# Kernel tuning notes

Hardware: AMD Instinct MI355X
Metric: run time of the kernel (lower is better)

## Reference

```python
import jax, jax.numpy as jnp
import numpy as np

EPS = 1e-5

def binarize(x):
    # binarize11: sign to {-1,+1} (0 maps to +1)
    return jnp.where(x >= 0, 1.0, -1.0).astype(x.dtype)

def batchnorm_train(x, gamma, beta):
    # training-mode BatchNorm1D: batch statistics over axis 0
    mean = jnp.mean(x, axis=0)
    var = jnp.var(x, axis=0)
    return gamma * (x - mean) * jax.lax.rsqrt(var + EPS) + beta

def setup_inputs() -> dict:
    key = jax.random.key(0)
    ks = jax.random.split(key, 16)
    x = jax.random.uniform(ks[0], (65536, 784), dtype=jnp.float32)  # MNIST-like pixels in [0,1]
    shapes = [(256, 784), (256, 256), (256, 256), (256, 256), (10, 256)]
    inp = {"x": x}
    for i, (o, ii) in enumerate(shapes):
        inp[f"w{i}"] = jax.random.normal(ks[1 + i], (o, ii), dtype=jnp.float32) * 0.05
        inp[f"gamma{i}"] = jnp.ones((o,), dtype=jnp.float32)
        inp[f"beta{i}"] = jnp.zeros((o,), dtype=jnp.float32)
    return inp

def reference(x, w0, w1, w2, w3, w4, gamma0, gamma1, gamma2, gamma3, gamma4,
              beta0, beta1, beta2, beta3, beta4):
    ws = [w0, w1, w2, w3, w4]
    gs = [gamma0, gamma1, gamma2, gamma3, gamma4]
    bs = [beta0, beta1, beta2, beta3, beta4]
    out = x - 0.5
    for k in range(5):
        a = binarize(out)                 # binarize activations
        wb = binarize(ws[k])              # binarize weights
        out = a @ wb.T                    # [B, out_k]
        out = batchnorm_train(out, gs[k], bs[k])
    # faithful to original: Softmax(dim=0) = softmax over the BATCH axis
    return jax.nn.softmax(out, axis=0)
```

## Files before the change

### kernel.cpp

```cpp
#include <hip/hip_runtime.h>
#include <cstdint>
#include <climits>
#include <cstddef>

typedef unsigned long long u64;

#define B_ROWS 65536
#define BN_EPS 1e-5


__global__ __launch_bounds__(256) void prep_all(
    const float* __restrict__ x, const float* __restrict__ w0,
    const float* __restrict__ w1, const float* __restrict__ w2,
    const float* __restrict__ w3, const float* __restrict__ w4,
    u64* __restrict__ bitsx, u64* __restrict__ wb0p, u64* __restrict__ wbTp,
    u64* __restrict__ w4b,
    long long* gsum, long long* gsq, int* gmin, int* gmax, double* colsum)
{
    const int lane = threadIdx.x & 63;
    const int wv   = threadIdx.x >> 6;
    const int b    = blockIdx.x;

    if (b < 2048) {
        const int gw = b * 4 + wv;
        for (int i = 0; i < 8; ++i) {
            const int row = gw * 8 + i;
            const float4* xr = (const float4*)(x + (size_t)row * 784);
#pragma unroll
            for (int cg = 0; cg < 3; ++cg) {
                const float4 f = xr[cg*64 + lane];
                const u64 e0 = __ballot(f.x >= 0.5f);
                const u64 e1 = __ballot(f.y >= 0.5f);
                const u64 e2 = __ballot(f.z >= 0.5f);
                const u64 e3 = __ballot(f.w >= 0.5f);
                if (lane == 0) {
                    bitsx[(size_t)(cg*4+0)*65536 + row] = e0;
                    bitsx[(size_t)(cg*4+1)*65536 + row] = e1;
                    bitsx[(size_t)(cg*4+2)*65536 + row] = e2;
                    bitsx[(size_t)(cg*4+3)*65536 + row] = e3;
                }
            }
            float4 f = make_float4(-1.f, -1.f, -1.f, -1.f);
            if (lane < 4) f = xr[192 + lane];
            const u64 e0 = __ballot(f.x >= 0.5f) & 0xF;
            const u64 e1 = __ballot(f.y >= 0.5f) & 0xF;
            const u64 e2 = __ballot(f.z >= 0.5f) & 0xF;
            const u64 e3 = __ballot(f.w >= 0.5f) & 0xF;
            if (lane == 0)
                bitsx[(size_t)12*65536 + row] = e0 | (e1 << 4) | (e2 << 8) | (e3 << 12);
        }
    } else if (b < 2112) {
        const int c = (b - 2048) * 4 + wv;
        const int pb = (c & 7) * 13;
        const int g  = c >> 3;
        const float4* row = (const float4*)(w0 + (size_t)c * 784);
#pragma unroll
        for (int cg = 0; cg < 3; ++cg) {
            const float4 f = row[cg*64 + lane];
            const u64 e0 = __ballot(f.x >= 0.0f);
            const u64 e1 = __ballot(f.y >= 0.0f);
            const u64 e2 = __ballot(f.z >= 0.0f);
            const u64 e3 = __ballot(f.w >= 0.0f);
            if (lane == 0) {
                wb0p[(pb + cg*4+0)*32 + g] = e0;
                wb0p[(pb + cg*4+1)*32 + g] = e1;
                wb0p[(pb + cg*4+2)*32 + g] = e2;
                wb0p[(pb + cg*4+3)*32 + g] = e3;
            }
        }
        float4 f = make_float4(-1.f, -1.f, -1.f, -1.f);
        if (lane < 4) f = row[192 + lane];
        const u64 e0 = __ballot(f.x >= 0.0f) & 0xF;
        const u64 e1 = __ballot(f.y >= 0.0f) & 0xF;
        const u64 e2 = __ballot(f.z >= 0.0f) & 0xF;
        const u64 e3 = __ballot(f.w >= 0.0f) & 0xF;
        if (lane == 0) wb0p[(pb + 12)*32 + g] = e0 | (e1 << 4) | (e2 << 8) | (e3 << 12);
    } else if (b < 2307) {
        const int idx = (b - 2112) * 4 + wv;
        if (idx < 768) {
            const int L = idx >> 8, c = idx & 255;
            const float* ws = (L == 0) ? w1 : (L == 1) ? w2 : w3;
            const float4 f = *(const float4*)(ws + (size_t)c * 256 + 4*lane);
            const u64 e0 = __ballot(f.x >= 0.0f);
            const u64 e1 = __ballot(f.y >= 0.0f);
            const u64 e2 = __ballot(f.z >= 0.0f);
            const u64 e3 = __ballot(f.w >= 0.0f);
            if (lane == 0) {
                const int pb = (c & 7) * 4;
                const int g  = c >> 3;
                wbTp[L*1024 + (pb+0)*32 + g] = e0;
                wbTp[L*1024 + (pb+1)*32 + g] = e1;
                wbTp[L*1024 + (pb+2)*32 + g] = e2;
                wbTp[L*1024 + (pb+3)*32 + g] = e3;
            }
        } else if (idx < 778) {
            const int c = idx - 768;
            const float4 f = *(const float4*)(w4 + (size_t)c * 256 + 4*lane);
            const u64 e0 = __ballot(f.x >= 0.0f);
            const u64 e1 = __ballot(f.y >= 0.0f);
            const u64 e2 = __ballot(f.z >= 0.0f);
            const u64 e3 = __ballot(f.w >= 0.0f);
            if (lane == 0) {
                w4b[c*4+0] = e0; w4b[c*4+1] = e1; w4b[c*4+2] = e2; w4b[c*4+3] = e3;
            }
        }
    } else {
        for (int i = threadIdx.x; i < 1040; i += 256) { gsum[i] = 0; gsq[i] = 0; }
        if (threadIdx.x < 16) {
            gmin[threadIdx.x] = INT_MAX;
            gmax[threadIdx.x] = INT_MIN;
            colsum[threadIdx.x] = 0.0;
        }
    }
}

__device__ __forceinline__ void bn_threshold(long long sv, long long qv,
    float gaf, float bef, int& sg, int& t)
{
    const double mean = (double)sv / (double)B_ROWS;
    double var = (double)qv / (double)B_ROWS - mean * mean;
    if (var < 0.0) var = 0.0;
    const double rs    = 1.0 / sqrt(var + BN_EPS);
    const double scale = (double)gaf * rs;
    const double bt    = (double)bef;
    if (scale > 0.0) {
        const double tt = fmin(fmax(mean - bt / scale, -1e6), 1e6);
        sg = 1; t = (int)ceil(tt);
    } else if (scale < 0.0) {
        const double tt = fmin(fmax(mean - bt / scale, -1e6), 1e6);
        sg = -1; t = (int)(-floor(tt));
    } else { sg = 0; t = (bt >= 0.0) ? INT_MIN : 1; }
}

template<int KW>
__device__ __forceinline__ void gemm_coal(const u64* __restrict__ sA,
    const u64* __restrict__ sWp, int K, int row0,
    short* __restrict__ vout, long long* gsumL, long long* gsqL,
    int* sS, int* sQ)
{
    const int tid = threadIdx.x;
    const int ct  = tid & 31;
    const int rt  = tid >> 5;

    unsigned p2[8][4];
#pragma unroll
    for (int j = 0; j < 8; ++j)
#pragma unroll
        for (int e2 = 0; e2 < 4; ++e2) p2[j][e2] = 0;

#pragma unroll 1
    for (int k = 0; k < KW; ++k) {
        u64 a[8];
#pragma unroll
        for (int j = 0; j < 8; ++j) a[j] = sA[k*128 + rt + 16*j];
        u64 w[8];
#pragma unroll
        for (int e = 0; e < 8; ++e) w[e] = sWp[(e*KW + k)*32 + ct];
#pragma unroll
        for (int j = 0; j < 8; ++j)
#pragma unroll
            for (int e2 = 0; e2 < 4; ++e2)
                p2[j][e2] += (unsigned)__popcll(a[j] ^ w[2*e2])
                           + ((unsigned)__popcll(a[j] ^ w[2*e2+1]) << 16);
    }

    int sS8[8], sQ8[8];
#pragma unroll
    for (int e = 0; e < 8; ++e) { sS8[e] = 0; sQ8[e] = 0; }

#pragma unroll
    for (int j = 0; j < 8; ++j) {
        const int r = row0 + rt + 16*j;
        unsigned pk[4];
#pragma unroll
        for (int e2 = 0; e2 < 4; ++e2) {
            const int v0 = K - 2 * (int)(p2[j][e2] & 0xFFFFu);
            const int v1 = K - 2 * (int)(p2[j][e2] >> 16);
            sS8[2*e2]   += v0; sQ8[2*e2]   += v0*v0;
            sS8[2*e2+1] += v1; sQ8[2*e2+1] += v1*v1;
            pk[e2] = (unsigned)(unsigned short)(short)v0
                   | ((unsigned)(unsigned short)(short)v1 << 16);
        }
        *(uint4*)(vout + (size_t)r * 256 + 8*ct) = make_uint4(pk[0], pk[1], pk[2], pk[3]);
    }

#pragma unroll
    for (int e = 0; e < 8; ++e) {
        sS8[e] += __shfl_xor(sS8[e], 32);
        sQ8[e] += __shfl_xor(sQ8[e], 32);
    }
    if ((tid & 63) < 32) {
#pragma unroll
        for (int e = 0; e < 8; ++e) {
            atomicAdd(&sS[8*ct + e], sS8[e]);
            atomicAdd(&sQ[8*ct + e], sQ8[e]);
        }
    }
    __syncthreads();
    if (tid < 256) {
        atomicAdd((u64*)&gsumL[tid], (u64)(long long)sS[tid]);
        atomicAdd((u64*)&gsqL[tid],  (u64)(long long)sQ[tid]);
    }
}

__global__ __launch_bounds__(512, 4) void layer0_kernel(
    const u64* __restrict__ bitsx, const u64* __restrict__ wb0p,
    short* __restrict__ v, long long* gsum, long long* gsq)
{
    __shared__ __align__(16) u64 sA[13*128];
    __shared__ __align__(16) u64 sWp[13*8*32];
    __shared__ int sS[256], sQ[256];
    const int tid  = threadIdx.x;
    const int row0 = blockIdx.x * 128;
    for (int i = tid; i < 13*128; i += 512)
        sA[i] = bitsx[(size_t)(i >> 7)*65536 + row0 + (i & 127)];
    for (int i = tid; i < 13*8*32; i += 512) sWp[i] = wb0p[i];
    if (tid < 256) { sS[tid] = 0; sQ[tid] = 0; }
    __syncthreads();
    gemm_coal<13>(sA, sWp, 784, row0, v, gsum, gsq, sS, sQ);
}

__global__ __launch_bounds__(512, 4) void layer_mid_kernel(
    short* v,
    const long long* __restrict__ gsumP, const long long* __restrict__ gsqP,
    const float* __restrict__ gaP, const float* __restrict__ beP,
    const u64* __restrict__ wbTpL, long long* gsumC, long long* gsqC)
{
    __shared__ __align__(16) u64 sA[4*128];
    __shared__ __align__(16) u64 sWp[4*8*32];
    __shared__ int sSgn[256], sThr[256];
    __shared__ int sS[256], sQ[256];
    const int tid  = threadIdx.x;
    const int lane = tid & 63;
    const int wv   = tid >> 6;
    const int row0 = blockIdx.x * 128;

    for (int i = tid; i < 4*8*32; i += 512) sWp[i] = wbTpL[i];
    if (tid < 256) {
        int sg, t;
        bn_threshold(gsumP[tid], gsqP[tid], gaP[tid], beP[tid], sg, t);
        sSgn[tid] = sg; sThr[tid] = t;
        sS[tid] = 0; sQ[tid] = 0;
    }
    __syncthreads();

    const int4 sg4 = *(const int4*)&sSgn[4*lane];
    const int4 th4 = *(const int4*)&sThr[4*lane];
    for (int i = 0; i < 16; ++i) {
        const int r = wv * 16 + i;
        const short4 vv = *(const short4*)(v + (size_t)(row0 + r)*256 + 4*lane);
        const u64 e0 = __ballot(sg4.x * (int)vv.x >= th4.x);
        const u64 e1 = __ballot(sg4.y * (int)vv.y >= th4.y);
        const u64 e2 = __ballot(sg4.z * (int)vv.z >= th4.z);
        const u64 e3 = __ballot(sg4.w * (int)vv.w >= th4.w);
        if (lane == 0) {
            sA[0*128 + r] = e0; sA[1*128 + r] = e1;
            sA[2*128 + r] = e2; sA[3*128 + r] = e3;
        }
    }
    __syncthreads();
    gemm_coal<4>(sA, sWp, 256, row0, v, gsumC, gsqC, sS, sQ);
}

__global__ __launch_bounds__(512) void layer4_kernel(
    const short* __restrict__ v,
    const long long* __restrict__ gsumP, const long long* __restrict__ gsqP,
    const float* __restrict__ gaP, const float* __restrict__ beP,
    const u64* __restrict__ w4b, short* __restrict__ v4,
    long long* gsum4, long long* gsq4, int* gmin, int* gmax)
{
    __shared__ int sSgn[256], sThr[256];
    __shared__ int sS[10], sQ[10], sMn[10], sMx[10];
    const int tid  = threadIdx.x;
    const int lane = tid & 63;
    const int wv   = tid >> 6;

    if (tid < 256) {
        int sg, t;
        bn_threshold(gsumP[tid], gsqP[tid], gaP[tid], beP[tid], sg, t);
        sSgn[tid] = sg; sThr[tid] = t;
    }
    if (tid < 10) { sS[tid] = 0; sQ[tid] = 0; sMn[tid] = INT_MAX; sMx[tid] = INT_MIN; }
    __syncthreads();

    const int4 sg4 = *(const int4*)&sSgn[4*lane];
    const int4 th4 = *(const int4*)&sThr[4*lane];

    u64 wc0 = 0, wc1 = 0, wc2 = 0, wc3 = 0;
    if (lane < 10) {
        wc0 = w4b[lane*4+0]; wc1 = w4b[lane*4+1];
        wc2 = w4b[lane*4+2]; wc3 = w4b[lane*4+3];
    }

    int accS = 0, accQ = 0, mn = INT_MAX, mx = INT_MIN;
    const int waveId = blockIdx.x * 8 + wv;
    const int r0 = waveId * 16;
#pragma unroll 2
    for (int i = 0; i < 16; ++i) {
        const int r = r0 + i;
        const short4 vv = *(const short4*)(v + (size_t)r*256 + 4*lane);
        const u64 e0 = __ballot(sg4.x * (int)vv.x >= th4.x);
        const u64 e1 = __ballot(sg4.y * (int)vv.y >= th4.y);
        const u64 e2 = __ballot(sg4.z * (int)vv.z >= th4.z);
        const u64 e3 = __ballot(sg4.w * (int)vv.w >= th4.w);
        if (lane < 10) {
            const int p = (int)__popcll(e0 ^ wc0) + (int)__popcll(e1 ^ wc1)
                        + (int)__popcll(e2 ^ wc2) + (int)__popcll(e3 ^ wc3);
            const int vr = 256 - 2*p;
            v4[(size_t)r*10 + lane] = (short)vr;
            accS += vr; accQ += vr*vr;
            mn = min(mn, vr); mx = max(mx, vr);
        }
    }
    if (lane < 10) {
        atomicAdd(&sS[lane], accS);
        atomicAdd(&sQ[lane], accQ);
        atomicMin(&sMn[lane], mn);
        atomicMax(&sMx[lane], mx);
    }
    __syncthreads();
    if (tid < 10) {
        atomicAdd((u64*)&gsum4[tid], (u64)(long long)sS[tid]);
        atomicAdd((u64*)&gsq4[tid],  (u64)(long long)sQ[tid]);
        atomicMin(&gmin[tid], sMn[tid]);
        atomicMax(&gmax[tid], sMx[tid]);
    }
}

__global__ __launch_bounds__(256) void colsum_kernel(
    const short* __restrict__ v4,
    const long long* __restrict__ gsum4, const long long* __restrict__ gsq4,
    const int* __restrict__ gmin, const int* __restrict__ gmax,
    const float* __restrict__ g4, const float* __restrict__ b4,
    double* zsg, double* zbg, double* colsum)
{
    __shared__ double sred[256];
    __shared__ double sZ[2];
    const int c     = blockIdx.x % 10;
    const int chunk = blockIdx.x / 10;
    const int tid   = threadIdx.x;
    if (tid == 0) {
        const double mean = (double)gsum4[c] / (double)B_ROWS;
        double var = (double)gsq4[c] / (double)B_ROWS - mean * mean;
        if (var < 0.0) var = 0.0;
        const double rs    = 1.0 / sqrt(var + BN_EPS);
        const double scale = (double)g4[c] * rs;
        const double bias  = (double)b4[c] - mean * scale;
        const double z1 = scale * (double)gmin[c] + bias;
        const double z2 = scale * (double)gmax[c] + bias;
        const double zb = bias - fmax(z1, z2);
        sZ[0] = scale; sZ[1] = zb;
        zsg[c] = scale; zbg[c] = zb;
    }
    __syncthreads();
    const double zs = sZ[0], zb = sZ[1];
    double acc = 0.0;
    const int r0 = chunk * 1024;
#pragma unroll
    for (int j = 0; j < 4; ++j) {
        const int r = r0 + j*256 + tid;
        acc += exp(zs * (double)v4[(size_t)r*10 + c] + zb);
    }
    sred[tid] = acc; __syncthreads();
    for (int s = 128; s > 0; s >>= 1) {
        if (tid < s) sred[tid] += sred[tid + s];
        __syncthreads();
    }
    if (tid == 0) atomicAdd(&colsum[c], sred[0]);
}

__global__ __launch_bounds__(256) void out_kernel(
    const short* __restrict__ v4, const double* __restrict__ zsg,
    const double* __restrict__ zbg, const double* __restrict__ colsum,
    float* __restrict__ out)
{
    const int idx = blockIdx.x * 256 + threadIdx.x;
    if (idx >= B_ROWS * 10) return;
    const int c = idx % 10;
    out[idx] = (float)(exp(zsg[c] * (double)v4[idx] + zbg[c]) / colsum[c]);
}

extern "C" void kernel_launch(void* const* d_in, const int* in_sizes, int n_in,
                              void* d_out, int out_size, void* d_ws, size_t ws_size,
                              hipStream_t stream)
{
    const float* x  = (const float*)d_in[0];
    const float* w0 = (const float*)d_in[1];
    const float* g0 = (const float*)d_in[2];
    const float* b0 = (const float*)d_in[3];
    const float* w1 = (const float*)d_in[4];
    const float* g1 = (const float*)d_in[5];
    const float* b1 = (const float*)d_in[6];
    const float* w2 = (const float*)d_in[7];
    const float* g2 = (const float*)d_in[8];
    const float* b2 = (const float*)d_in[9];
    const float* w3 = (const float*)d_in[10];
    const float* g3 = (const float*)d_in[11];
    const float* b3 = (const float*)d_in[12];
    const float* w4 = (const float*)d_in[13];
    const float* g4 = (const float*)d_in[14];
    const float* b4 = (const float*)d_in[15];

    char* p = (char*)d_ws;
    auto alloc = [&](size_t bytes) -> char* {
        char* r = p;
        p += (bytes + 255) & ~(size_t)255;
        return r;
    };
    u64*       bitsx  = (u64*)alloc(13ull*65536*8);
    u64*       wb0p   = (u64*)alloc(13*8*32*8);
    u64*       wbTp   = (u64*)alloc(3*1024*8);
    u64*       w4b    = (u64*)alloc(40*8);
    short*     v      = (short*)alloc(65536ull*256*2);
    short*     v4     = (short*)alloc(65536ull*10*2);
    long long* gsum   = (long long*)alloc(1040*8);
    long long* gsq    = (long long*)alloc(1040*8);
    int*       gmin   = (int*)alloc(16*4);
    int*       gmax   = (int*)alloc(16*4);
    double*    colsum = (double*)alloc(16*8);
    double*    zsg    = (double*)alloc(16*8);
    double*    zbg    = (double*)alloc(16*8);
    float*     out    = (float*)d_out;

    long long* gsum4 = gsum + 1024;
    long long* gsq4  = gsq  + 1024;

    prep_all<<<2308, 256, 0, stream>>>(x, w0, w1, w2, w3, w4,
                                       bitsx, wb0p, wbTp, w4b,
                                       gsum, gsq, gmin, gmax, colsum);

    layer0_kernel<<<512, 512, 0, stream>>>(bitsx, wb0p, v, gsum, gsq);

    layer_mid_kernel<<<512, 512, 0, stream>>>(v, gsum, gsq, g0, b0,
                                              wbTp + 0*1024, gsum + 256, gsq + 256);
    layer_mid_kernel<<<512, 512, 0, stream>>>(v, gsum + 256, gsq + 256, g1, b1,
                                              wbTp + 1*1024, gsum + 512, gsq + 512);
    layer_mid_kernel<<<512, 512, 0, stream>>>(v, gsum + 512, gsq + 512, g2, b2,
                                              wbTp + 2*1024, gsum + 768, gsq + 768);

    layer4_kernel<<<512, 512, 0, stream>>>(v, gsum + 768, gsq + 768, g3, b3,
                                           w4b, v4, gsum4, gsq4, gmin, gmax);

    colsum_kernel<<<640, 256, 0, stream>>>(v4, gsum4, gsq4, gmin, gmax, g4, b4,
                                           zsg, zbg, colsum);

    out_kernel<<<2560, 256, 0, stream>>>(v4, zsg, zbg, colsum, out);
}
```

Before: 207.3 us.

## Fuse input binarization into layer0 GEMM and shrink blocks to 32 rows

```diff
diff --git a/kernel.cpp b/kernel.cpp
--- a/kernel.cpp
+++ b/kernel.cpp
@@ -9,48 +9,19 @@
 #define BN_EPS 1e-5
 
 
-__global__ __launch_bounds__(256) void prep_all(
-    const float* __restrict__ x, const float* __restrict__ w0,
-    const float* __restrict__ w1, const float* __restrict__ w2,
-    const float* __restrict__ w3, const float* __restrict__ w4,
-    u64* __restrict__ bitsx, u64* __restrict__ wb0p, u64* __restrict__ wbTp,
-    u64* __restrict__ w4b,
+__global__ __launch_bounds__(256) void prep_w(
+    const float* __restrict__ w0, const float* __restrict__ w1,
+    const float* __restrict__ w2, const float* __restrict__ w3,
+    const float* __restrict__ w4,
+    u64* __restrict__ wb0p, u64* __restrict__ wbTp, u64* __restrict__ w4b,
     long long* gsum, long long* gsq, int* gmin, int* gmax, double* colsum)
 {
     const int lane = threadIdx.x & 63;
     const int wv   = threadIdx.x >> 6;
     const int b    = blockIdx.x;
 
-    if (b < 2048) {
-        const int gw = b * 4 + wv;
-        for (int i = 0; i < 8; ++i) {
-            const int row = gw * 8 + i;
-            const float4* xr = (const float4*)(x + (size_t)row * 784);
-#pragma unroll
-            for (int cg = 0; cg < 3; ++cg) {
-                const float4 f = xr[cg*64 + lane];
-                const u64 e0 = __ballot(f.x >= 0.5f);
-                const u64 e1 = __ballot(f.y >= 0.5f);
-                const u64 e2 = __ballot(f.z >= 0.5f);
-                const u64 e3 = __ballot(f.w >= 0.5f);
-                if (lane == 0) {
-                    bitsx[(size_t)(cg*4+0)*65536 + row] = e0;
-                    bitsx[(size_t)(cg*4+1)*65536 + row] = e1;
-                    bitsx[(size_t)(cg*4+2)*65536 + row] = e2;
-                    bitsx[(size_t)(cg*4+3)*65536 + row] = e3;
-                }
-            }
-            float4 f = make_float4(-1.f, -1.f, -1.f, -1.f);
-            if (lane < 4) f = xr[192 + lane];
-            const u64 e0 = __ballot(f.x >= 0.5f) & 0xF;
-            const u64 e1 = __ballot(f.y >= 0.5f) & 0xF;
-            const u64 e2 = __ballot(f.z >= 0.5f) & 0xF;
-            const u64 e3 = __ballot(f.w >= 0.5f) & 0xF;
-            if (lane == 0)
-                bitsx[(size_t)12*65536 + row] = e0 | (e1 << 4) | (e2 << 8) | (e3 << 12);
-        }
-    } else if (b < 2112) {
-        const int c = (b - 2048) * 4 + wv;
+    if (b < 64) {
+        const int c  = b * 4 + wv;
         const int pb = (c & 7) * 13;
         const int g  = c >> 3;
         const float4* row = (const float4*)(w0 + (size_t)c * 784);
@@ -75,33 +46,33 @@
         const u64 e2 = __ballot(f.z >= 0.0f) & 0xF;
         const u64 e3 = __ballot(f.w >= 0.0f) & 0xF;
         if (lane == 0) wb0p[(pb + 12)*32 + g] = e0 | (e1 << 4) | (e2 << 8) | (e3 << 12);
-    } else if (b < 2307) {
-        const int idx = (b - 2112) * 4 + wv;
-        if (idx < 768) {
-            const int L = idx >> 8, c = idx & 255;
-            const float* ws = (L == 0) ? w1 : (L == 1) ? w2 : w3;
-            const float4 f = *(const float4*)(ws + (size_t)c * 256 + 4*lane);
-            const u64 e0 = __ballot(f.x >= 0.0f);
-            const u64 e1 = __ballot(f.y >= 0.0f);
-            const u64 e2 = __ballot(f.z >= 0.0f);
-            const u64 e3 = __ballot(f.w >= 0.0f);
-            if (lane == 0) {
-                const int pb = (c & 7) * 4;
-                const int g  = c >> 3;
-                wbTp[L*1024 + (pb+0)*32 + g] = e0;
-                wbTp[L*1024 + (pb+1)*32 + g] = e1;
-                wbTp[L*1024 + (pb+2)*32 + g] = e2;
-                wbTp[L*1024 + (pb+3)*32 + g] = e3;
-            }
-        } else if (idx < 778) {
-            const int c = idx - 768;
+    } else if (b < 256) {
+        const int idx = (b - 64) * 4 + wv;
+        const int L = idx >> 8, c = idx & 255;
+        const float* ws = (L == 0) ? w1 : (L == 1) ? w2 : w3;
+        const float4 f = *(const float4*)(ws + (size_t)c * 256 + 4*lane);
+        const u64 e0 = __ballot(f.x >= 0.0f);
+        const u64 e1 = __ballot(f.y >= 0.0f);
+        const u64 e2 = __ballot(f.z >= 0.0f);
+        const u64 e3 = __ballot(f.w >= 0.0f);
+        if (lane == 0) {
+            const int pb = (c & 7) * 4;
+            const int g  = c >> 3;
+            wbTp[L*1024 + (pb+0)*32 + g] = e0;
+            wbTp[L*1024 + (pb+1)*32 + g] = e1;
+            wbTp[L*1024 + (pb+2)*32 + g] = e2;
+            wbTp[L*1024 + (pb+3)*32 + g] = e3;
+        }
+    } else if (b == 256) {
+        for (int c = wv; c < 10; c += 4) {
             const float4 f = *(const float4*)(w4 + (size_t)c * 256 + 4*lane);
             const u64 e0 = __ballot(f.x >= 0.0f);
             const u64 e1 = __ballot(f.y >= 0.0f);
             const u64 e2 = __ballot(f.z >= 0.0f);
             const u64 e3 = __ballot(f.w >= 0.0f);
             if (lane == 0) {
-                w4b[c*4+0] = e0; w4b[c*4+1] = e1; w4b[c*4+2] = e2; w4b[c*4+3] = e3;
+                w4b[c*4+0] = e0; w4b[c*4+1] = e1;
+                w4b[c*4+2] = e2; w4b[c*4+3] = e3;
             }
         }
     } else {
@@ -133,7 +104,7 @@
 }
 
 template<int KW>
-__device__ __forceinline__ void gemm_coal(const u64* __restrict__ sA,
+__device__ __forceinline__ void gemm32(const u64* __restrict__ sA,
     const u64* __restrict__ sWp, int K, int row0,
     short* __restrict__ vout, long long* gsumL, long long* gsqL,
     int* sS, int* sQ)
@@ -142,42 +113,42 @@
     const int ct  = tid & 31;
     const int rt  = tid >> 5;
 
-    unsigned p2[8][4];
-#pragma unroll
-    for (int j = 0; j < 8; ++j)
+    unsigned p2[4][4];
+#pragma unroll
+    for (int j = 0; j < 4; ++j)
 #pragma unroll
         for (int e2 = 0; e2 < 4; ++e2) p2[j][e2] = 0;
 
 #pragma unroll 1
     for (int k = 0; k < KW; ++k) {
-        u64 a[8];
-#pragma unroll
-        for (int j = 0; j < 8; ++j) a[j] = sA[k*128 + rt + 16*j];
+        u64 a[4];
+#pragma unroll
+        for (int j = 0; j < 4; ++j) a[j] = sA[k*32 + rt + 8*j];
         u64 w[8];
 #pragma unroll
         for (int e = 0; e < 8; ++e) w[e] = sWp[(e*KW + k)*32 + ct];
 #pragma unroll
-        for (int j = 0; j < 8; ++j)
+        for (int j = 0; j < 4; ++j)
 #pragma unroll
             for (int e2 = 0; e2 < 4; ++e2)
                 p2[j][e2] += (unsigned)__popcll(a[j] ^ w[2*e2])
                            + ((unsigned)__popcll(a[j] ^ w[2*e2+1]) << 16);
     }
 
-    int sS8[8], sQ8[8];
-#pragma unroll
-    for (int e = 0; e < 8; ++e) { sS8[e] = 0; sQ8[e] = 0; }
-
-#pragma unroll
-    for (int j = 0; j < 8; ++j) {
-        const int r = row0 + rt + 16*j;
+    int s8[8], q8[8];
+#pragma unroll
+    for (int e = 0; e < 8; ++e) { s8[e] = 0; q8[e] = 0; }
+
+#pragma unroll
+    for (int j = 0; j < 4; ++j) {
+        const int r = row0 + rt + 8*j;
         unsigned pk[4];
 #pragma unroll
         for (int e2 = 0; e2 < 4; ++e2) {
             const int v0 = K - 2 * (int)(p2[j][e2] & 0xFFFFu);
             const int v1 = K - 2 * (int)(p2[j][e2] >> 16);
-            sS8[2*e2]   += v0; sQ8[2*e2]   += v0*v0;
-            sS8[2*e2+1] += v1; sQ8[2*e2+1] += v1*v1;
+            s8[2*e2]   += v0; q8[2*e2]   += v0*v0;
+            s8[2*e2+1] += v1; q8[2*e2+1] += v1*v1;
             pk[e2] = (unsigned)(unsigned short)(short)v0
                    | ((unsigned)(unsigned short)(short)v1 << 16);
         }
@@ -186,57 +157,83 @@
 
 #pragma unroll
     for (int e = 0; e < 8; ++e) {
-        sS8[e] += __shfl_xor(sS8[e], 32);
-        sQ8[e] += __shfl_xor(sQ8[e], 32);
+        s8[e] += __shfl_xor(s8[e], 32);
+        q8[e] += __shfl_xor(q8[e], 32);
     }
     if ((tid & 63) < 32) {
 #pragma unroll
         for (int e = 0; e < 8; ++e) {
-            atomicAdd(&sS[8*ct + e], sS8[e]);
-            atomicAdd(&sQ[8*ct + e], sQ8[e]);
-        }
-    }
-    __syncthreads();
-    if (tid < 256) {
-        atomicAdd((u64*)&gsumL[tid], (u64)(long long)sS[tid]);
-        atomicAdd((u64*)&gsqL[tid],  (u64)(long long)sQ[tid]);
-    }
-}
-
-__global__ __launch_bounds__(512, 4) void layer0_kernel(
-    const u64* __restrict__ bitsx, const u64* __restrict__ wb0p,
+            atomicAdd(&sS[8*ct + e], s8[e]);
+            atomicAdd(&sQ[8*ct + e], q8[e]);
+        }
+    }
+    __syncthreads();
+    atomicAdd((u64*)&gsumL[tid], (u64)(long long)sS[tid]);
+    atomicAdd((u64*)&gsqL[tid],  (u64)(long long)sQ[tid]);
+}
+
+__global__ __launch_bounds__(256, 5) void fused0(
+    const float* __restrict__ x, const u64* __restrict__ wb0p,
     short* __restrict__ v, long long* gsum, long long* gsq)
 {
-    __shared__ __align__(16) u64 sA[13*128];
+    __shared__ __align__(16) u64 sA[13*32];
     __shared__ __align__(16) u64 sWp[13*8*32];
     __shared__ int sS[256], sQ[256];
     const int tid  = threadIdx.x;
-    const int row0 = blockIdx.x * 128;
-    for (int i = tid; i < 13*128; i += 512)
-        sA[i] = bitsx[(size_t)(i >> 7)*65536 + row0 + (i & 127)];
-    for (int i = tid; i < 13*8*32; i += 512) sWp[i] = wb0p[i];
-    if (tid < 256) { sS[tid] = 0; sQ[tid] = 0; }
-    __syncthreads();
-    gemm_coal<13>(sA, sWp, 784, row0, v, gsum, gsq, sS, sQ);
-}
-
-__global__ __launch_bounds__(512, 4) void layer_mid_kernel(
+    const int lane = tid & 63;
+    const int wv   = tid >> 6;
+    const int row0 = blockIdx.x * 32;
+
+    for (int i = tid; i < 13*8*32; i += 256) sWp[i] = wb0p[i];
+    sS[tid] = 0; sQ[tid] = 0;
+
+#pragma unroll 2
+    for (int i = 0; i < 8; ++i) {
+        const int r   = wv * 8 + i;
+        const float4* xr = (const float4*)(x + (size_t)(row0 + r) * 784);
+#pragma unroll
+        for (int cg = 0; cg < 3; ++cg) {
+            const float4 f = xr[cg*64 + lane];
+            const u64 e0 = __ballot(f.x >= 0.5f);
+            const u64 e1 = __ballot(f.y >= 0.5f);
+            const u64 e2 = __ballot(f.z >= 0.5f);
+            const u64 e3 = __ballot(f.w >= 0.5f);
+            if (lane == 0) {
+                sA[(cg*4+0)*32 + r] = e0;
+                sA[(cg*4+1)*32 + r] = e1;
+                sA[(cg*4+2)*32 + r] = e2;
+                sA[(cg*4+3)*32 + r] = e3;
+            }
+        }
+        float4 f = make_float4(-1.f, -1.f, -1.f, -1.f);
+        if (lane < 4) f = xr[192 + lane];
+        const u64 e0 = __ballot(f.x >= 0.5f) & 0xF;
+        const u64 e1 = __ballot(f.y >= 0.5f) & 0xF;
+        const u64 e2 = __ballot(f.z >= 0.5f) & 0xF;
+        const u64 e3 = __ballot(f.w >= 0.5f) & 0xF;
+        if (lane == 0) sA[12*32 + r] = e0 | (e1 << 4) | (e2 << 8) | (e3 << 12);
+    }
+    __syncthreads();
+    gemm32<13>(sA, sWp, 784, row0, v, gsum, gsq, sS, sQ);
+}
+
+__global__ __launch_bounds__(256, 6) void layer_mid(
     short* v,
     const long long* __restrict__ gsumP, const long long* __restrict__ gsqP,
     const float* __restrict__ gaP, const float* __restrict__ beP,
     const u64* __restrict__ wbTpL, long long* gsumC, long long* gsqC)
 {
-    __shared__ __align__(16) u64 sA[4*128];
+    __shared__ __align__(16) u64 sA[4*32];
     __shared__ __align__(16) u64 sWp[4*8*32];
     __shared__ int sSgn[256], sThr[256];
     __shared__ int sS[256], sQ[256];
     const int tid  = threadIdx.x;
     const int lane = tid & 63;
     const int wv   = tid >> 6;
-    const int row0 = blockIdx.x * 128;
-
-    for (int i = tid; i < 4*8*32; i += 512) sWp[i] = wbTpL[i];
-    if (tid < 256) {
+    const int row0 = blockIdx.x * 32;
+
+    for (int i = tid; i < 4*8*32; i += 256) sWp[i] = wbTpL[i];
+    {
         int sg, t;
         bn_threshold(gsumP[tid], gsqP[tid], gaP[tid], beP[tid], sg, t);
         sSgn[tid] = sg; sThr[tid] = t;
@@ -246,20 +243,21 @@
 
     const int4 sg4 = *(const int4*)&sSgn[4*lane];
     const int4 th4 = *(const int4*)&sThr[4*lane];
-    for (int i = 0; i < 16; ++i) {
-        const int r = wv * 16 + i;
+#pragma unroll 2
+    for (int i = 0; i < 8; ++i) {
+        const int r = wv * 8 + i;
         const short4 vv = *(const short4*)(v + (size_t)(row0 + r)*256 + 4*lane);
         const u64 e0 = __ballot(sg4.x * (int)vv.x >= th4.x);
         const u64 e1 = __ballot(sg4.y * (int)vv.y >= th4.y);
         const u64 e2 = __ballot(sg4.z * (int)vv.z >= th4.z);
         const u64 e3 = __ballot(sg4.w * (int)vv.w >= th4.w);
         if (lane == 0) {
-            sA[0*128 + r] = e0; sA[1*128 + r] = e1;
-            sA[2*128 + r] = e2; sA[3*128 + r] = e3;
-        }
-    }
-    __syncthreads();
-    gemm_coal<4>(sA, sWp, 256, row0, v, gsumC, gsqC, sS, sQ);
+            sA[0*32 + r] = e0; sA[1*32 + r] = e1;
+            sA[2*32 + r] = e2; sA[3*32 + r] = e3;
+        }
+    }
+    __syncthreads();
+    gemm32<4>(sA, sWp, 256, row0, v, gsumC, gsqC, sS, sQ);
 }
 
 __global__ __launch_bounds__(512) void layer4_kernel(
@@ -359,7 +357,7 @@
 #pragma unroll
     for (int j = 0; j < 4; ++j) {
         const int r = r0 + j*256 + tid;
-        acc += exp(zs * (double)v4[(size_t)r*10 + c] + zb);
+        acc += (double)expf((float)(zs * (double)v4[(size_t)r*10 + c] + zb));
     }
     sred[tid] = acc; __syncthreads();
     for (int s = 128; s > 0; s >>= 1) {
@@ -377,7 +375,8 @@
     const int idx = blockIdx.x * 256 + threadIdx.x;
     if (idx >= B_ROWS * 10) return;
     const int c = idx % 10;
-    out[idx] = (float)(exp(zsg[c] * (double)v4[idx] + zbg[c]) / colsum[c]);
+    const float e = expf((float)(zsg[c] * (double)v4[idx] + zbg[c]));
+    out[idx] = (float)((double)e / colsum[c]);
 }
 
 extern "C" void kernel_launch(void* const* d_in, const int* in_sizes, int n_in,
@@ -407,7 +406,6 @@
         p += (bytes + 255) & ~(size_t)255;
         return r;
     };
-    u64*       bitsx  = (u64*)alloc(13ull*65536*8);
     u64*       wb0p   = (u64*)alloc(13*8*32*8);
     u64*       wbTp   = (u64*)alloc(3*1024*8);
     u64*       w4b    = (u64*)alloc(40*8);
@@ -425,18 +423,17 @@
     long long* gsum4 = gsum + 1024;
     long long* gsq4  = gsq  + 1024;
 
-    prep_all<<<2308, 256, 0, stream>>>(x, w0, w1, w2, w3, w4,
-                                       bitsx, wb0p, wbTp, w4b,
-                                       gsum, gsq, gmin, gmax, colsum);
-
-    layer0_kernel<<<512, 512, 0, stream>>>(bitsx, wb0p, v, gsum, gsq);
-
-    layer_mid_kernel<<<512, 512, 0, stream>>>(v, gsum, gsq, g0, b0,
-                                              wbTp + 0*1024, gsum + 256, gsq + 256);
-    layer_mid_kernel<<<512, 512, 0, stream>>>(v, gsum + 256, gsq + 256, g1, b1,
-                                              wbTp + 1*1024, gsum + 512, gsq + 512);
-    layer_mid_kernel<<<512, 512, 0, stream>>>(v, gsum + 512, gsq + 512, g2, b2,
-                                              wbTp + 2*1024, gsum + 768, gsq + 768);
+    prep_w<<<258, 256, 0, stream>>>(w0, w1, w2, w3, w4, wb0p, wbTp, w4b,
+                                    gsum, gsq, gmin, gmax, colsum);
+
+    fused0<<<2048, 256, 0, stream>>>(x, wb0p, v, gsum, gsq);
+
+    layer_mid<<<2048, 256, 0, stream>>>(v, gsum, gsq, g0, b0,
+                                        wbTp + 0*1024, gsum + 256, gsq + 256);
+    layer_mid<<<2048, 256, 0, stream>>>(v, gsum + 256, gsq + 256, g1, b1,
+                                        wbTp + 1*1024, gsum + 512, gsq + 512);
+    layer_mid<<<2048, 256, 0, stream>>>(v, gsum + 512, gsq + 512, g2, b2,
+                                        wbTp + 2*1024, gsum + 768, gsq + 768);
 
     layer4_kernel<<<512, 512, 0, stream>>>(v, gsum + 768, gsq + 768, g3, b3,
                                            w4b, v4, gsum4, gsq4, gmin, gmax);
```

Result: slower. 295.1 us (+42.4%).
